# Kernel optimization log

Hardware: AMD Instinct MI355X
Metric: run time of the kernel (lower is better)

The kernel has to match this reference:

```python
import jax, jax.numpy as jnp
import numpy as np

IMG = 128
FX, FY, CX, CY = 588.03, 587.07, 320.0, 240.0
FLIP = 1.0
SAMPLE = 1024  # sample_num in Img2pcl
N_VERTS = 778


def setup_inputs() -> dict:
    key = jax.random.key(0)
    ks = jax.random.split(key, 6)
    B = 64
    real = jax.random.uniform(ks[0], (B, 1, IMG, IMG), jnp.float32)   # normalized depth in [0,1)
    synth = jax.random.uniform(ks[1], (B, 1, IMG, IMG), jnp.float32)  # unused by forward
    verts = jax.random.normal(ks[2], (B, N_VERTS, 3), jnp.float32)
    faces = jax.random.randint(ks[3], (1538, 3), 0, N_VERTS, jnp.int32)  # unused by forward
    center = jax.random.normal(ks[4], (B, 3), jnp.float32) * 0.1 + jnp.array([0.0, 0.0, 400.0], jnp.float32)
    # crop matrix must be invertible: identity plus small perturbation
    M = jnp.eye(3, dtype=jnp.float32)[None] + 0.1 * jax.random.normal(ks[5], (B, 3, 3), jnp.float32)
    cube = jnp.full((B, 3), 250.0, jnp.float32)
    return dict(real=real, synth=synth, verts=verts, faces=faces, center=center, M=M, cube=cube)


def _img2pcl(real, center, M, cube):
    """Vectorized Img2pcl: normalized (u,v,d) -> normalized xyz for every pixel, plus valid mask."""
    B = real.shape[0]
    # input already IMG x IMG so F.interpolate is identity
    img = real[:, 0]                                   # [B,H,W]
    t = 2.0 * jnp.arange(IMG, dtype=jnp.float32) / (IMG - 1.0) - 1.0
    mesh_x = jnp.broadcast_to(t[:, None], (IMG, IMG))  # varies along rows (v)
    mesh_y = jnp.broadcast_to(t[None, :], (IMG, IMG))  # varies along cols (u)
    uvd = jnp.stack([
        jnp.broadcast_to(mesh_y, (B, IMG, IMG)),
        jnp.broadcast_to(mesh_x, (B, IMG, IMG)),
        img,
    ], axis=-1).reshape(B, IMG * IMG, 3)               # [B,P,3]
    # unnormalize uv and depth
    uv = (uvd[..., :2] + 1.0) * (IMG / 2.0)
    d = uvd[..., 2] * (cube[:, None, 2] / 2.0) + center[:, None, 2]   # [B,P]
    # get_trans_points with M^{-1}
    M_inv = jnp.linalg.inv(M)                          # [B,3,3]
    h = jnp.concatenate([uv, jnp.ones_like(uv[..., :1])], axis=-1)    # [B,P,3]
    uv_w = jnp.einsum('bij,bpj->bpi', M_inv, h)[..., :2]
    # pointsImgTo3D (pinhole back-projection)
    x = (uv_w[..., 0] - CX) * d / FX
    y = FLIP * (uv_w[..., 1] - CY) * d / FY
    xyz = jnp.stack([x, y, d], axis=-1)                # [B,P,3]
    xyz_n = (xyz - center[:, None, :]) / (cube[:, None, :] / 2.0)
    mask = img.reshape(B, -1) <= 0.99                  # valid (foreground) pixels
    return xyz_n, mask


def reference(real, synth, verts, faces, center, M, cube):
    xyz, mask = _img2pcl(real, center, M, cube)
    # torch.multinomial(uniform weights, SAMPLE, without replacement) over valid pixels
    # == Gumbel top-k over the masked candidate set (jit-compatible, fixed shapes)
    u = jax.random.uniform(jax.random.key(1), mask.shape)
    gumbel = -jnp.log(-jnp.log(u + 1e-20) + 1e-20)
    score = jnp.where(mask, gumbel, -jnp.inf)
    _, idx = jax.lax.top_k(score, SAMPLE)              # [B,SAMPLE]
    pcl1 = jnp.take_along_axis(xyz, idx[..., None], axis=1)  # [B,SAMPLE,3]
    # chamfer distance (pytorch3d-style: mean-reduced squared-dist NN, both directions)
    d2 = jnp.sum((pcl1[:, :, None, :] - verts[:, None, :, :]) ** 2, axis=-1)  # [B,SAMPLE,V]
    loss = d2.min(axis=2).mean() + d2.min(axis=1).mean()
    return loss
```

## Files before the change

### kernel.cpp

```cpp
#include <hip/hip_runtime.h>
#include <stdint.h>
#include <math.h>

#define NPIX   16384
#define SAMPLE 1024
#define NV     778
#define BATCH  64

__device__ __forceinline__ uint32_t rotl32(uint32_t v, int r) {
  return (v << r) | (v >> (32 - r));
}

__device__ __forceinline__ void threefry2x32(uint32_t ks0, uint32_t ks1,
                                             uint32_t x0, uint32_t x1,
                                             uint32_t& o0, uint32_t& o1) {
  uint32_t ks2 = ks0 ^ ks1 ^ 0x1BD11BDAu;
  x0 += ks0; x1 += ks1;
#define TF_R(r) { x0 += x1; x1 = rotl32(x1, (r)); x1 ^= x0; }
  TF_R(13) TF_R(15) TF_R(26) TF_R(6)
  x0 += ks1; x1 += ks2 + 1u;
  TF_R(17) TF_R(29) TF_R(16) TF_R(24)
  x0 += ks2; x1 += ks0 + 2u;
  TF_R(13) TF_R(15) TF_R(26) TF_R(6)
  x0 += ks0; x1 += ks1 + 3u;
  TF_R(17) TF_R(29) TF_R(16) TF_R(24)
  x0 += ks1; x1 += ks2 + 4u;
  TF_R(13) TF_R(15) TF_R(26) TF_R(6)
  x0 += ks2; x1 += ks0 + 5u;
#undef TF_R
  o0 = x0; o1 = x1;
}

__device__ __forceinline__ float waveReduceSum(float v) {
#pragma unroll
  for (int off = 32; off > 0; off >>= 1) v += __shfl_down(v, off, 64);
  return v;
}

__global__ __launch_bounds__(256) void score_kernel(
    const float4* __restrict__ real4, uint4* __restrict__ uval4) {
  const int i = blockIdx.x * 256 + threadIdx.x;
  float4 im = real4[i];
  const uint32_t base = (uint32_t)i * 4u;
  uint32_t h0, h1;
  uint4 o;
  threefry2x32(0u, 1u, 0u, base + 0u, h0, h1);
  o.x = (im.x <= 0.99f) ? (((h0 ^ h1) >> 9) + 1u) : 0u;
  threefry2x32(0u, 1u, 0u, base + 1u, h0, h1);
  o.y = (im.y <= 0.99f) ? (((h0 ^ h1) >> 9) + 1u) : 0u;
  threefry2x32(0u, 1u, 0u, base + 2u, h0, h1);
  o.z = (im.z <= 0.99f) ? (((h0 ^ h1) >> 9) + 1u) : 0u;
  threefry2x32(0u, 1u, 0u, base + 3u, h0, h1);
  o.w = (im.w <= 0.99f) ? (((h0 ^ h1) >> 9) + 1u) : 0u;
  uval4[i] = o;
}

__global__ __launch_bounds__(1024) void select_kernel(
    const uint32_t* __restrict__ uval,
    const float* __restrict__ real,
    const float* __restrict__ center,
    const float* __restrict__ M,
    const float* __restrict__ cube,
    float4* __restrict__ pcl4) {
  const int b = blockIdx.x;
  const int tid = threadIdx.x;
  const int lane = tid & 63;
  const int wv = tid >> 6;

  __shared__ uint32_t hist[512];
  __shared__ uint32_t wt[8], offs[8];
  __shared__ uint64_t cand[512];
  __shared__ float sh_minv[6], sh_c[3], sh_hb[3];
  __shared__ uint32_t sh_cnt, sh_ccnt, sh_bstar, sh_above;

  if (tid == 0) {
    const float* m = M + (size_t)b * 9;
    float m00=m[0], m01=m[1], m02=m[2];
    float m10=m[3], m11=m[4], m12=m[5];
    float m20=m[6], m21=m[7], m22=m[8];
    float c00 = m11*m22 - m12*m21;
    float c10 = m12*m20 - m10*m22;
    float c20 = m10*m21 - m11*m20;
    float det = m00*c00 + m01*c10 + m02*c20;
    float id = 1.0f / det;
    sh_minv[0] = c00 * id;
    sh_minv[1] = (m02*m21 - m01*m22) * id;
    sh_minv[2] = (m01*m12 - m02*m11) * id;
    sh_minv[3] = c10 * id;
    sh_minv[4] = (m00*m22 - m02*m20) * id;
    sh_minv[5] = (m02*m10 - m00*m12) * id;
    sh_c[0] = center[b*3+0]; sh_c[1] = center[b*3+1]; sh_c[2] = center[b*3+2];
    sh_hb[0] = cube[b*3+0]*0.5f; sh_hb[1] = cube[b*3+1]*0.5f; sh_hb[2] = cube[b*3+2]*0.5f;
    sh_cnt = 0; sh_ccnt = 0;
  }
  if (tid < 512) hist[tid] = 0;

  const uint4* mb4 = (const uint4*)(uval + (size_t)b * NPIX);
  uint32_t uv[16];
#pragma unroll
  for (int e4 = 0; e4 < 4; ++e4) {
    uint4 q = mb4[e4 * 1024 + tid];
    uv[e4*4+0] = q.x; uv[e4*4+1] = q.y; uv[e4*4+2] = q.z; uv[e4*4+3] = q.w;
  }
  __syncthreads();

#pragma unroll
  for (int e = 0; e < 16; ++e)
    if (uv[e]) atomicAdd(&hist[(uv[e] - 1u) >> 14], 1u);
  __syncthreads();

  uint32_t cnt = 0, sfx = 0;
  if (tid < 512) {
    cnt = hist[tid];
    sfx = cnt;
#pragma unroll
    for (int off = 1; off < 64; off <<= 1) {
      uint32_t u = __shfl_down(sfx, off, 64);
      if (lane + off < 64) sfx += u;
    }
    if (lane == 0) wt[wv] = sfx;
  }
  __syncthreads();
  if (tid < 8) {
    uint32_t t = wt[tid], s = t;
#pragma unroll
    for (int off = 1; off < 8; off <<= 1) {
      uint32_t u = __shfl_down(s, off, 64);
      if (tid + off < 8) s += u;
    }
    offs[tid] = s - t;
  }
  __syncthreads();
  if (tid < 512) {
    uint32_t tot = sfx + offs[wv];
    uint32_t above = tot - cnt;
    if (tot >= SAMPLE && above < SAMPLE && cnt > 0) {
      sh_bstar = (uint32_t)tid;
      sh_above = above;
    }
  }
  __syncthreads();
  const int bstar = (int)sh_bstar;
  const uint32_t kneed = SAMPLE - sh_above;

  const float* rb = real + (size_t)b * NPIX;
  float4* ob = pcl4 + (size_t)b * SAMPLE;
  auto emit = [&](int p, uint32_t slot) {
    int i = p >> 7, j = p & 127;
    float tj = (2.0f * (float)j) / 127.0f - 1.0f;
    float ti = (2.0f * (float)i) / 127.0f - 1.0f;
    float u0 = (tj + 1.0f) * 64.0f;
    float u1 = (ti + 1.0f) * 64.0f;
    float d  = rb[p] * sh_hb[2] + sh_c[2];
    float w0 = sh_minv[0]*u0 + sh_minv[1]*u1 + sh_minv[2];
    float w1 = sh_minv[3]*u0 + sh_minv[4]*u1 + sh_minv[5];
    float x = (w0 - 320.0f) * d / 588.03f;
    float y = (w1 - 240.0f) * d / 587.07f;
    float4 o;
    o.x = (x - sh_c[0]) / sh_hb[0];
    o.y = (y - sh_c[1]) / sh_hb[1];
    o.z = (d - sh_c[2]) / sh_hb[2];
    o.w = 0.0f;
    ob[slot] = o;
  };

#pragma unroll
  for (int e = 0; e < 16; ++e) {
    uint32_t v = uv[e];
    int p = (e >> 2) * 4096 + (tid << 2) + (e & 3);
    int bk = v ? (int)((v - 1u) >> 14) : -1;
    bool hi = (bk > bstar);
    unsigned long long m = __ballot(hi);
    if (m) {
      int leader = __ffsll((unsigned long long)m) - 1;
      uint32_t base;
      if (lane == leader) base = atomicAdd(&sh_cnt, (uint32_t)__popcll(m));
      base = __shfl(base, leader, 64);
      if (hi) emit(p, base + (uint32_t)__popcll(m & ((1ull << lane) - 1ull)));
    }
    bool eqb = (bk == bstar);
    unsigned long long m2 = __ballot(eqb);
    if (m2) {
      int leader = __ffsll((unsigned long long)m2) - 1;
      uint32_t cb;
      if (lane == leader) cb = atomicAdd(&sh_ccnt, (uint32_t)__popcll(m2));
      cb = __shfl(cb, leader, 64);
      if (eqb) {
        uint32_t ci = cb + (uint32_t)__popcll(m2 & ((1ull << lane) - 1ull));
        if (ci < 512) cand[ci] = ((uint64_t)v << 14) | (uint64_t)(16383 - p);
      }
    }
  }
  __syncthreads();

  uint32_t c = sh_ccnt; if (c > 512) c = 512;
  if (tid < 64) {
    for (uint32_t basei = 0; basei < c; basei += 64) {
      uint32_t i = basei + (uint32_t)lane;
      bool act = (i < c);
      uint64_t ki = act ? cand[i] : 0ull;
      uint32_t rank = 0;
      for (uint32_t j2 = 0; j2 < c; ++j2) rank += (cand[j2] > ki) ? 1u : 0u;
      bool sel = act && (rank < kneed);
      unsigned long long m = __ballot(sel);
      if (m) {
        int leader = __ffsll((unsigned long long)m) - 1;
        uint32_t base;
        if (lane == leader) base = atomicAdd(&sh_cnt, (uint32_t)__popcll(m));
        base = __shfl(base, leader, 64);
        if (sel) {
          int p = 16383 - (int)(ki & 0x3FFFull);
          emit(p, base + (uint32_t)__popcll(m & ((1ull << lane) - 1ull)));
        }
      }
    }
  }
}

#define NA_BLOCKS 512
#define NB_SLICES 7
#define NB_BLOCKS (BATCH * NB_SLICES)

__global__ __launch_bounds__(256, 4) void dist_kernel(
    const float* __restrict__ verts,
    const float4* __restrict__ pcl4,
    float* __restrict__ partials) {
  __shared__ __align__(16) uint8_t shbuf[20480];
  __shared__ float red[4];
  const int blk = blockIdx.x;
  const int tid = threadIdx.x;
  const int s = tid >> 5;
  const int g = tid & 31;
  float val = 0.0f;

  if (blk < NA_BLOCKS) {
    const int b = blk >> 3, slice = blk & 7;
    float4* sv4 = (float4*)shbuf;
    float* pmin = (float*)(shbuf + 12448);
    const float* vb = verts + (size_t)b * NV * 3;
    for (int v = tid; v < NV; v += 256) {
      float4 t;
      t.x = vb[v*3]; t.y = vb[v*3+1]; t.z = vb[v*3+2]; t.w = 0.0f;
      sv4[v] = t;
    }
    const float4* pb = pcl4 + (size_t)b * SAMPLE + slice * 128;
    float px[4], py[4], pz[4], mn[4];
#pragma unroll
    for (int j = 0; j < 4; ++j) {
      float4 q = pb[j * 32 + g];
      px[j] = q.x; py[j] = q.y; pz[j] = q.z; mn[j] = INFINITY;
    }
    __syncthreads();
    const int vs = s * 98;
    const int ve = (vs + 98 < NV) ? vs + 98 : NV;
    for (int v = vs; v < ve; ++v) {
      float4 vv = sv4[v];
#pragma unroll
      for (int j = 0; j < 4; ++j) {
        float dx = px[j] - vv.x, dy = py[j] - vv.y, dz = pz[j] - vv.z;
        float d2 = dx*dx + dy*dy + dz*dz;
        mn[j] = fminf(mn[j], d2);
      }
    }
#pragma unroll
    for (int j = 0; j < 4; ++j) pmin[s * 128 + j * 32 + g] = mn[j];
    __syncthreads();
    if (tid < 128) {
      float m = pmin[tid];
#pragma unroll
      for (int ss = 1; ss < 8; ++ss) m = fminf(m, pmin[ss * 128 + tid]);
      val = m;
    }
  } else {
    const int bb = blk - NA_BLOCKS;
    const int b = bb / NB_SLICES, slice = bb % NB_SLICES;
    float4* sp4 = (float4*)shbuf;
    float* vmin = (float*)(shbuf + 16384);
    const float4* pcb = pcl4 + (size_t)b * SAMPLE;
    for (int i = tid; i < SAMPLE; i += 256) sp4[i] = pcb[i];
    const float* vb = verts + (size_t)b * NV * 3;
    const int vbase = slice * 128;
    float vx[4], vy[4], vz[4], mn[4];
#pragma unroll
    for (int j = 0; j < 4; ++j) {
      int v = vbase + j * 32 + g;
      int vc = (v < NV) ? v : 0;
      vx[j] = vb[vc*3]; vy[j] = vb[vc*3+1]; vz[j] = vb[vc*3+2];
      mn[j] = INFINITY;
    }
    __syncthreads();
    const int ps = s * 128;
    for (int i = 0; i < 128; ++i) {
      float4 pt = sp4[ps + i];
#pragma unroll
      for (int j = 0; j < 4; ++j) {
        float dx = pt.x - vx[j], dy = pt.y - vy[j], dz = pt.z - vz[j];
        float d2 = dx*dx + dy*dy + dz*dz;
        mn[j] = fminf(mn[j], d2);
      }
    }
#pragma unroll
    for (int j = 0; j < 4; ++j) vmin[s * 128 + j * 32 + g] = mn[j];
    __syncthreads();
    if (tid < 128 && (vbase + tid) < NV) {
      float m = vmin[tid];
#pragma unroll
      for (int ss = 1; ss < 8; ++ss) m = fminf(m, vmin[ss * 128 + tid]);
      val = m;
    }
  }

  float r = waveReduceSum(val);
  if ((tid & 63) == 0) red[tid >> 6] = r;
  __syncthreads();
  if (tid == 0) partials[blk] = red[0] + red[1] + red[2] + red[3];
}

__global__ __launch_bounds__(1024) void finalize_kernel(
    const float* __restrict__ partials, float* __restrict__ out) {
  const int tid = threadIdx.x;
  __shared__ float redA[16], redB[16];
  float v = (tid < NA_BLOCKS + NB_BLOCKS) ? partials[tid] : 0.0f;
  float a  = (tid < NA_BLOCKS) ? v : 0.0f;
  float bs = (tid >= NA_BLOCKS) ? v : 0.0f;
  a  = waveReduceSum(a);
  bs = waveReduceSum(bs);
  int w = tid >> 6, lane = tid & 63;
  if (lane == 0) { redA[w] = a; redB[w] = bs; }
  __syncthreads();
  if (tid == 0) {
    float A = 0.0f, B = 0.0f;
#pragma unroll
    for (int i = 0; i < 16; ++i) { A += redA[i]; B += redB[i]; }
    out[0] = A / (float)(BATCH * SAMPLE) + B / (float)(BATCH * NV);
  }
}

extern "C" void kernel_launch(void* const* d_in, const int* in_sizes, int n_in,
                              void* d_out, int out_size, void* d_ws, size_t ws_size,
                              hipStream_t stream) {
  const float* real   = (const float*)d_in[0];
  const float* verts  = (const float*)d_in[2];
  const float* center = (const float*)d_in[4];
  const float* M      = (const float*)d_in[5];
  const float* cube   = (const float*)d_in[6];

  uint32_t* uval  = (uint32_t*)d_ws;
  float4* pcl4    = (float4*)((char*)d_ws + (4u << 20));
  float* partials = (float*)((char*)d_ws + (5u << 20));
  float* out = (float*)d_out;

  score_kernel<<<dim3(BATCH * NPIX / 4 / 256), dim3(256), 0, stream>>>(
      (const float4*)real, (uint4*)uval);
  select_kernel<<<dim3(BATCH), dim3(1024), 0, stream>>>(
      uval, real, center, M, cube, pcl4);
  dist_kernel<<<dim3(NA_BLOCKS + NB_BLOCKS), dim3(256), 0, stream>>>(
      verts, pcl4, partials);
  finalize_kernel<<<dim3(1), dim3(1024), 0, stream>>>(partials, out);
}
```

Measured before the change: 120.2 us.

## Fuse RNG scoring into select, expand distance algebra, drop finalize kernel

Threefry hashing and masking move into the select kernel, so the uval buffer is no longer written and read back and the separate score launch goes away. The selected depth now comes from registers instead of a second gather from global memory. The distance kernels switch to the expanded form |p|^2 - 2p·v + |v|^2, which takes three FMAs per pair, and pre-scale the inputs in shared memory. The finalize kernel is replaced by a float atomicAdd into the output after a memset. This makes the sum order nondeterministic and adds cancellation error from the expanded distance. The select kernel now does all the threefry work with only 64 blocks, which may leave the GPU underused.

```diff
diff --git a/kernel.cpp b/kernel.cpp
--- a/kernel.cpp
+++ b/kernel.cpp
@@ -7,15 +7,17 @@
 #define NV     778
 #define BATCH  64
 
+#define A_SCALE (1.0f / (float)(BATCH * SAMPLE))
+#define B_SCALE (1.0f / (float)(BATCH * NV))
+
 __device__ __forceinline__ uint32_t rotl32(uint32_t v, int r) {
   return (v << r) | (v >> (32 - r));
 }
 
-__device__ __forceinline__ void threefry2x32(uint32_t ks0, uint32_t ks1,
-                                             uint32_t x0, uint32_t x1,
-                                             uint32_t& o0, uint32_t& o1) {
+__device__ __forceinline__ uint32_t threefry_bits(uint32_t g) {
+  uint32_t ks0 = 0u, ks1 = 1u;
   uint32_t ks2 = ks0 ^ ks1 ^ 0x1BD11BDAu;
-  x0 += ks0; x1 += ks1;
+  uint32_t x0 = 0u + ks0, x1 = g + ks1;
 #define TF_R(r) { x0 += x1; x1 = rotl32(x1, (r)); x1 ^= x0; }
   TF_R(13) TF_R(15) TF_R(26) TF_R(6)
   x0 += ks1; x1 += ks2 + 1u;
@@ -28,7 +30,7 @@
   TF_R(13) TF_R(15) TF_R(26) TF_R(6)
   x0 += ks2; x1 += ks0 + 5u;
 #undef TF_R
-  o0 = x0; o1 = x1;
+  return x0 ^ x1;
 }
 
 __device__ __forceinline__ float waveReduceSum(float v) {
@@ -37,27 +39,8 @@
   return v;
 }
 
-__global__ __launch_bounds__(256) void score_kernel(
-    const float4* __restrict__ real4, uint4* __restrict__ uval4) {
-  const int i = blockIdx.x * 256 + threadIdx.x;
-  float4 im = real4[i];
-  const uint32_t base = (uint32_t)i * 4u;
-  uint32_t h0, h1;
-  uint4 o;
-  threefry2x32(0u, 1u, 0u, base + 0u, h0, h1);
-  o.x = (im.x <= 0.99f) ? (((h0 ^ h1) >> 9) + 1u) : 0u;
-  threefry2x32(0u, 1u, 0u, base + 1u, h0, h1);
-  o.y = (im.y <= 0.99f) ? (((h0 ^ h1) >> 9) + 1u) : 0u;
-  threefry2x32(0u, 1u, 0u, base + 2u, h0, h1);
-  o.z = (im.z <= 0.99f) ? (((h0 ^ h1) >> 9) + 1u) : 0u;
-  threefry2x32(0u, 1u, 0u, base + 3u, h0, h1);
-  o.w = (im.w <= 0.99f) ? (((h0 ^ h1) >> 9) + 1u) : 0u;
-  uval4[i] = o;
-}
-
 __global__ __launch_bounds__(1024) void select_kernel(
-    const uint32_t* __restrict__ uval,
-    const float* __restrict__ real,
+    const float4* __restrict__ real4,
     const float* __restrict__ center,
     const float* __restrict__ M,
     const float* __restrict__ cube,
@@ -70,6 +53,7 @@
   __shared__ uint32_t hist[512];
   __shared__ uint32_t wt[8], offs[8];
   __shared__ uint64_t cand[512];
+  __shared__ float candrv[512];
   __shared__ float sh_minv[6], sh_c[3], sh_hb[3];
   __shared__ uint32_t sh_cnt, sh_ccnt, sh_bstar, sh_above;
 
@@ -95,12 +79,18 @@
   }
   if (tid < 512) hist[tid] = 0;
 
-  const uint4* mb4 = (const uint4*)(uval + (size_t)b * NPIX);
   uint32_t uv[16];
+  float    rv[16];
+  const float4* rb4 = real4 + (size_t)b * (NPIX / 4);
 #pragma unroll
   for (int e4 = 0; e4 < 4; ++e4) {
-    uint4 q = mb4[e4 * 1024 + tid];
-    uv[e4*4+0] = q.x; uv[e4*4+1] = q.y; uv[e4*4+2] = q.z; uv[e4*4+3] = q.w;
+    float4 im = rb4[e4 * 1024 + tid];
+    uint32_t base = (uint32_t)(b * NPIX + e4 * 4096) + (uint32_t)(tid << 2);
+    rv[e4*4+0] = im.x; rv[e4*4+1] = im.y; rv[e4*4+2] = im.z; rv[e4*4+3] = im.w;
+    uv[e4*4+0] = (im.x <= 0.99f) ? ((threefry_bits(base + 0u) >> 9) + 1u) : 0u;
+    uv[e4*4+1] = (im.y <= 0.99f) ? ((threefry_bits(base + 1u) >> 9) + 1u) : 0u;
+    uv[e4*4+2] = (im.z <= 0.99f) ? ((threefry_bits(base + 2u) >> 9) + 1u) : 0u;
+    uv[e4*4+3] = (im.w <= 0.99f) ? ((threefry_bits(base + 3u) >> 9) + 1u) : 0u;
   }
   __syncthreads();
 
@@ -143,15 +133,14 @@
   const int bstar = (int)sh_bstar;
   const uint32_t kneed = SAMPLE - sh_above;
 
-  const float* rb = real + (size_t)b * NPIX;
   float4* ob = pcl4 + (size_t)b * SAMPLE;
-  auto emit = [&](int p, uint32_t slot) {
+  auto emit = [&](int p, float depth01, uint32_t slot) {
     int i = p >> 7, j = p & 127;
     float tj = (2.0f * (float)j) / 127.0f - 1.0f;
     float ti = (2.0f * (float)i) / 127.0f - 1.0f;
     float u0 = (tj + 1.0f) * 64.0f;
     float u1 = (ti + 1.0f) * 64.0f;
-    float d  = rb[p] * sh_hb[2] + sh_c[2];
+    float d  = depth01 * sh_hb[2] + sh_c[2];
     float w0 = sh_minv[0]*u0 + sh_minv[1]*u1 + sh_minv[2];
     float w1 = sh_minv[3]*u0 + sh_minv[4]*u1 + sh_minv[5];
     float x = (w0 - 320.0f) * d / 588.03f;
@@ -176,7 +165,7 @@
       uint32_t base;
       if (lane == leader) base = atomicAdd(&sh_cnt, (uint32_t)__popcll(m));
       base = __shfl(base, leader, 64);
-      if (hi) emit(p, base + (uint32_t)__popcll(m & ((1ull << lane) - 1ull)));
+      if (hi) emit(p, rv[e], base + (uint32_t)__popcll(m & ((1ull << lane) - 1ull)));
     }
     bool eqb = (bk == bstar);
     unsigned long long m2 = __ballot(eqb);
@@ -187,7 +176,10 @@
       cb = __shfl(cb, leader, 64);
       if (eqb) {
         uint32_t ci = cb + (uint32_t)__popcll(m2 & ((1ull << lane) - 1ull));
-        if (ci < 512) cand[ci] = ((uint64_t)v << 14) | (uint64_t)(16383 - p);
+        if (ci < 512) {
+          cand[ci] = ((uint64_t)v << 14) | (uint64_t)(16383 - p);
+          candrv[ci] = rv[e];
+        }
       }
     }
   }
@@ -210,7 +202,7 @@
         base = __shfl(base, leader, 64);
         if (sel) {
           int p = 16383 - (int)(ki & 0x3FFFull);
-          emit(p, base + (uint32_t)__popcll(m & ((1ull << lane) - 1ull)));
+          emit(p, candrv[i], base + (uint32_t)__popcll(m & ((1ull << lane) - 1ull)));
         }
       }
     }
@@ -224,8 +216,8 @@
 __global__ __launch_bounds__(256, 4) void dist_kernel(
     const float* __restrict__ verts,
     const float4* __restrict__ pcl4,
-    float* __restrict__ partials) {
-  __shared__ __align__(16) uint8_t shbuf[20480];
+    float* __restrict__ out) {
+  __shared__ __align__(16) uint8_t shbuf[20992];
   __shared__ float red[4];
   const int blk = blockIdx.x;
   const int tid = threadIdx.x;
@@ -237,18 +229,22 @@
     const int b = blk >> 3, slice = blk & 7;
     float4* sv4 = (float4*)shbuf;
     float* pmin = (float*)(shbuf + 12448);
+    float* npl  = (float*)(shbuf + 16544);
     const float* vb = verts + (size_t)b * NV * 3;
     for (int v = tid; v < NV; v += 256) {
+      float x = vb[v*3], y = vb[v*3+1], z = vb[v*3+2];
       float4 t;
-      t.x = vb[v*3]; t.y = vb[v*3+1]; t.z = vb[v*3+2]; t.w = 0.0f;
+      t.x = -2.0f*x; t.y = -2.0f*y; t.z = -2.0f*z; t.w = x*x + y*y + z*z;
       sv4[v] = t;
     }
     const float4* pb = pcl4 + (size_t)b * SAMPLE + slice * 128;
-    float px[4], py[4], pz[4], mn[4];
+    float px[4], py[4], pz[4], np[4], mn[4];
 #pragma unroll
     for (int j = 0; j < 4; ++j) {
       float4 q = pb[j * 32 + g];
-      px[j] = q.x; py[j] = q.y; pz[j] = q.z; mn[j] = INFINITY;
+      px[j] = q.x; py[j] = q.y; pz[j] = q.z;
+      np[j] = q.x*q.x + q.y*q.y + q.z*q.z;
+      mn[j] = INFINITY;
     }
     __syncthreads();
     const int vs = s * 98;
@@ -257,35 +253,45 @@
       float4 vv = sv4[v];
 #pragma unroll
       for (int j = 0; j < 4; ++j) {
-        float dx = px[j] - vv.x, dy = py[j] - vv.y, dz = pz[j] - vv.z;
-        float d2 = dx*dx + dy*dy + dz*dz;
-        mn[j] = fminf(mn[j], d2);
+        float t = fmaf(pz[j], vv.z, fmaf(py[j], vv.y, fmaf(px[j], vv.x, vv.w)));
+        mn[j] = fminf(mn[j], t);
       }
     }
 #pragma unroll
-    for (int j = 0; j < 4; ++j) pmin[s * 128 + j * 32 + g] = mn[j];
+    for (int j = 0; j < 4; ++j) {
+      pmin[s * 128 + j * 32 + g] = mn[j];
+      if (s == 0) npl[j * 32 + g] = np[j];
+    }
     __syncthreads();
     if (tid < 128) {
       float m = pmin[tid];
 #pragma unroll
       for (int ss = 1; ss < 8; ++ss) m = fminf(m, pmin[ss * 128 + tid]);
-      val = m;
+      val = (m + npl[tid]) * A_SCALE;
     }
   } else {
     const int bb = blk - NA_BLOCKS;
     const int b = bb / NB_SLICES, slice = bb % NB_SLICES;
     float4* sp4 = (float4*)shbuf;
     float* vmin = (float*)(shbuf + 16384);
+    float* nvl  = (float*)(shbuf + 20480);
     const float4* pcb = pcl4 + (size_t)b * SAMPLE;
-    for (int i = tid; i < SAMPLE; i += 256) sp4[i] = pcb[i];
+    for (int i = tid; i < SAMPLE; i += 256) {
+      float4 q = pcb[i];
+      float4 t;
+      t.x = -2.0f*q.x; t.y = -2.0f*q.y; t.z = -2.0f*q.z;
+      t.w = q.x*q.x + q.y*q.y + q.z*q.z;
+      sp4[i] = t;
+    }
     const float* vb = verts + (size_t)b * NV * 3;
     const int vbase = slice * 128;
-    float vx[4], vy[4], vz[4], mn[4];
+    float vx[4], vy[4], vz[4], nv[4], mn[4];
 #pragma unroll
     for (int j = 0; j < 4; ++j) {
       int v = vbase + j * 32 + g;
       int vc = (v < NV) ? v : 0;
       vx[j] = vb[vc*3]; vy[j] = vb[vc*3+1]; vz[j] = vb[vc*3+2];
+      nv[j] = vx[j]*vx[j] + vy[j]*vy[j] + vz[j]*vz[j];
       mn[j] = INFINITY;
     }
     __syncthreads();
@@ -294,46 +300,28 @@
       float4 pt = sp4[ps + i];
 #pragma unroll
       for (int j = 0; j < 4; ++j) {
-        float dx = pt.x - vx[j], dy = pt.y - vy[j], dz = pt.z - vz[j];
-        float d2 = dx*dx + dy*dy + dz*dz;
-        mn[j] = fminf(mn[j], d2);
+        float t = fmaf(vz[j], pt.z, fmaf(vy[j], pt.y, fmaf(vx[j], pt.x, pt.w)));
+        mn[j] = fminf(mn[j], t);
       }
     }
 #pragma unroll
-    for (int j = 0; j < 4; ++j) vmin[s * 128 + j * 32 + g] = mn[j];
+    for (int j = 0; j < 4; ++j) {
+      vmin[s * 128 + j * 32 + g] = mn[j];
+      if (s == 0) nvl[j * 32 + g] = nv[j];
+    }
     __syncthreads();
     if (tid < 128 && (vbase + tid) < NV) {
       float m = vmin[tid];
 #pragma unroll
       for (int ss = 1; ss < 8; ++ss) m = fminf(m, vmin[ss * 128 + tid]);
-      val = m;
+      val = (m + nvl[tid]) * B_SCALE;
     }
   }
 
   float r = waveReduceSum(val);
   if ((tid & 63) == 0) red[tid >> 6] = r;
   __syncthreads();
-  if (tid == 0) partials[blk] = red[0] + red[1] + red[2] + red[3];
-}
-
-__global__ __launch_bounds__(1024) void finalize_kernel(
-    const float* __restrict__ partials, float* __restrict__ out) {
-  const int tid = threadIdx.x;
-  __shared__ float redA[16], redB[16];
-  float v = (tid < NA_BLOCKS + NB_BLOCKS) ? partials[tid] : 0.0f;
-  float a  = (tid < NA_BLOCKS) ? v : 0.0f;
-  float bs = (tid >= NA_BLOCKS) ? v : 0.0f;
-  a  = waveReduceSum(a);
-  bs = waveReduceSum(bs);
-  int w = tid >> 6, lane = tid & 63;
-  if (lane == 0) { redA[w] = a; redB[w] = bs; }
-  __syncthreads();
-  if (tid == 0) {
-    float A = 0.0f, B = 0.0f;
-#pragma unroll
-    for (int i = 0; i < 16; ++i) { A += redA[i]; B += redB[i]; }
-    out[0] = A / (float)(BATCH * SAMPLE) + B / (float)(BATCH * NV);
-  }
+  if (tid == 0) atomicAdd(out, red[0] + red[1] + red[2] + red[3]);
 }
 
 extern "C" void kernel_launch(void* const* d_in, const int* in_sizes, int n_in,
@@ -345,16 +333,12 @@
   const float* M      = (const float*)d_in[5];
   const float* cube   = (const float*)d_in[6];
 
-  uint32_t* uval  = (uint32_t*)d_ws;
-  float4* pcl4    = (float4*)((char*)d_ws + (4u << 20));
-  float* partials = (float*)((char*)d_ws + (5u << 20));
+  float4* pcl4 = (float4*)d_ws;
   float* out = (float*)d_out;
 
-  score_kernel<<<dim3(BATCH * NPIX / 4 / 256), dim3(256), 0, stream>>>(
-      (const float4*)real, (uint4*)uval);
+  hipMemsetAsync(out, 0, sizeof(float), stream);
   select_kernel<<<dim3(BATCH), dim3(1024), 0, stream>>>(
-      uval, real, center, M, cube, pcl4);
+      (const float4*)real, center, M, cube, pcl4);
   dist_kernel<<<dim3(NA_BLOCKS + NB_BLOCKS), dim3(256), 0, stream>>>(
-      verts, pcl4, partials);
-  finalize_kernel<<<dim3(1), dim3(1024), 0, stream>>>(partials, out);
-}
+      verts, pcl4, out);
+}
```

Result: no change. 119.7 us (-0.4%).
